# Kernel optimization log

Measured on AMD Instinct MI355X. Metric: run time of the kernel, lower is better.

Reference implementation:

```python
import jax, jax.numpy as jnp
import numpy as np
from jax import lax

# ---- module hyperparams (match init_kwargs and mamba_ssm Mamba2 defaults) ----
D_MODEL = 768
D_STATE = 64
D_CONV = 4
EXPAND = 2
HEADDIM = 64  # Mamba2 default
D_INNER = EXPAND * D_MODEL          # 1536
NHEADS = D_INNER // HEADDIM         # 24
NGROUPS = 1
CONV_DIM = D_INNER + 2 * NGROUPS * D_STATE          # 1664
D_IN_PROJ = 2 * D_INNER + 2 * NGROUPS * D_STATE + NHEADS  # 3224
BSZ, SEQ = 2, 512
EPS = 1e-5


def setup_inputs() -> dict:
    key = jax.random.key(0)
    ks = jax.random.split(key, 12)
    def n(k, shape, s):
        return jax.random.normal(k, shape, jnp.float32) * s
    x = n(ks[0], (BSZ, SEQ, D_MODEL), 1.0)
    in_proj_w = n(ks[1], (D_IN_PROJ, D_MODEL), D_MODEL ** -0.5)
    conv_w = n(ks[2], (CONV_DIM, D_CONV), D_CONV ** -0.5)
    conv_b = jnp.zeros((CONV_DIM,), jnp.float32)
    # dt_bias = softplus^{-1}(dt) with dt log-uniform in [1e-3, 1e-1] (Mamba2 init)
    dt = jnp.exp(jax.random.uniform(ks[3], (NHEADS,), jnp.float32,
                                    minval=np.log(1e-3), maxval=np.log(1e-1)))
    dt_bias = dt + jnp.log(-jnp.expm1(-dt))
    A_log = jnp.log(jax.random.uniform(ks[4], (NHEADS,), jnp.float32, minval=1.0, maxval=16.0))
    D_param = jnp.ones((NHEADS,), jnp.float32)
    norm_w = jnp.ones((D_INNER,), jnp.float32)
    out_proj_w = n(ks[5], (D_MODEL, D_INNER), D_INNER ** -0.5)
    ln1_w = jnp.ones((D_MODEL,), jnp.float32); ln1_b = jnp.zeros((D_MODEL,), jnp.float32)
    ln2_w = jnp.ones((D_MODEL,), jnp.float32); ln2_b = jnp.zeros((D_MODEL,), jnp.float32)
    ff_w1 = n(ks[6], (4 * D_MODEL, D_MODEL), D_MODEL ** -0.5)
    ff_b1 = jnp.zeros((4 * D_MODEL,), jnp.float32)
    ff_w2 = n(ks[7], (D_MODEL, 4 * D_MODEL), (4 * D_MODEL) ** -0.5)
    ff_b2 = jnp.zeros((D_MODEL,), jnp.float32)
    return dict(x=x, in_proj_w=in_proj_w, conv_w=conv_w, conv_b=conv_b,
                dt_bias=dt_bias, A_log=A_log, D_param=D_param, norm_w=norm_w,
                out_proj_w=out_proj_w, ln1_w=ln1_w, ln1_b=ln1_b,
                ln2_w=ln2_w, ln2_b=ln2_b, ff_w1=ff_w1, ff_b1=ff_b1,
                ff_w2=ff_w2, ff_b2=ff_b2)


def layernorm(x, w, b):
    mu = jnp.mean(x, -1, keepdims=True)
    xc = x - mu
    var = jnp.mean(xc * xc, -1, keepdims=True)
    return xc * lax.rsqrt(var + EPS) * w + b


def mamba2(xn, in_proj_w, conv_w, conv_b, dt_bias, A_log, D_param, norm_w, out_proj_w):
    b, l, _ = xn.shape
    zxbcdt = xn @ in_proj_w.T  # [b, l, D_IN_PROJ]
    z = zxbcdt[..., :D_INNER]
    xBC = zxbcdt[..., D_INNER:D_INNER + CONV_DIM]
    dt = zxbcdt[..., D_INNER + CONV_DIM:]
    # causal depthwise conv over time on xBC
    xc = lax.conv_general_dilated(xBC.transpose(0, 2, 1), conv_w[:, None, :], (1,),
                                  [(D_CONV - 1, 0)], dimension_numbers=('NCH', 'OIH', 'NCH'),
                                  feature_group_count=CONV_DIM)
    xBC = jax.nn.silu((xc + conv_b[None, :, None]).transpose(0, 2, 1))
    xs = xBC[..., :D_INNER].reshape(b, l, NHEADS, HEADDIM)
    Bm = xBC[..., D_INNER:D_INNER + D_STATE]   # [b, l, n]  (ngroups=1)
    Cm = xBC[..., D_INNER + D_STATE:]          # [b, l, n]
    dt = jax.nn.softplus(dt + dt_bias)         # [b, l, h]
    dA = jnp.exp(dt * (-jnp.exp(A_log)))       # [b, l, h]
    dBx = jnp.einsum('blh,bln,blhp->blhpn', dt, Bm, xs)
    def step(h, inp):
        dA_t, dBx_t = inp                      # [b,h], [b,h,p,n]
        h = dA_t[:, :, None, None] * h + dBx_t
        return h, h
    _, hs = lax.scan(step, jnp.zeros((b, NHEADS, HEADDIM, D_STATE), xn.dtype),
                     (dA.transpose(1, 0, 2), dBx.transpose(1, 0, 2, 3, 4)))
    y = jnp.einsum('lbhpn,bln->blhp', hs, Cm) + D_param[None, None, :, None] * xs
    y = y.reshape(b, l, D_INNER) * jax.nn.silu(z)   # gated RMSNorm (norm_before_gate=False)
    y = y * lax.rsqrt(jnp.mean(y * y, -1, keepdims=True) + EPS) * norm_w
    return y @ out_proj_w.T


def reference(x, in_proj_w, conv_w, conv_b, dt_bias, A_log, D_param, norm_w,
              out_proj_w, ln1_w, ln1_b, ln2_w, ln2_b, ff_w1, ff_b1, ff_w2, ff_b2):
    residual = x
    xn = layernorm(x, ln1_w, ln1_b)
    mp = (in_proj_w, conv_w, conv_b, dt_bias, A_log, D_param, norm_w, out_proj_w)
    out_f = mamba2(xn, *mp)
    out_b = jnp.flip(mamba2(jnp.flip(xn, 1), *mp), 1)
    m = layernorm(out_f + out_b, ln2_w, ln2_b)
    ff = jax.nn.gelu(m @ ff_w1.T + ff_b1, approximate=False) @ ff_w2.T + ff_b2
    return ff + residual
```

## Files before the change

### kernel.cpp

```cpp
#include <hip/hip_runtime.h>
#include <hip/hip_bf16.h>
#include <math.h>

#define SEQ     512
#define BSZ     2
#define ROWS    (BSZ*SEQ)
#define DMODEL  768
#define DINNER  1536
#define DSTATE  64
#define NHEADS  24
#define HEADDIM 64
#define CONVDIM 1664
#define DINPROJ 3224
#define DFF     3072
#define EPSF    1e-5f

typedef __attribute__((ext_vector_type(8))) short s16x8;
typedef __attribute__((ext_vector_type(4))) float f32x4;

__device__ __forceinline__ float b2f(const __hip_bfloat16 v){ return __bfloat162float(v); }
__device__ __forceinline__ __hip_bfloat16 f2b(float v){ return __float2bfloat16(v); }
__device__ __forceinline__ ushort f2bu(float v){
  union { __hip_bfloat16 b; ushort u; } c; c.b = __float2bfloat16(v); return c.u;
}
__device__ __forceinline__ float u2f(ushort u){ return __uint_as_float(((uint)u) << 16); }

__device__ __forceinline__ void gload16(const void* g, void* l){
  __builtin_amdgcn_global_load_lds((__attribute__((address_space(1))) const void*)g,
                                   (__attribute__((address_space(3))) void*)l, 16, 0, 0);
}

__device__ __forceinline__ float block_sum256(float v, float* sh){
  #pragma unroll
  for (int off = 32; off > 0; off >>= 1) v += __shfl_down(v, off, 64);
  int w = threadIdx.x >> 6;
  if ((threadIdx.x & 63) == 0) sh[w] = v;
  __syncthreads();
  float t = sh[0] + sh[1] + sh[2] + sh[3];
  __syncthreads();
  return t;
}

__global__ __launch_bounds__(256) void zerof_kernel(float* out, int n){
  int i = blockIdx.x*256 + threadIdx.x;
  if (i < n) out[i] = 0.f;
}

__global__ __launch_bounds__(256) void prep_kernel(const float* __restrict__ w0,
    const float* __restrict__ w1, const float* __restrict__ w2,
    const float* __restrict__ w3, ushort* __restrict__ o,
    int n0, int n1, int n2, int n3, int wblocks,
    const float* __restrict__ xin, const float* __restrict__ lnw,
    const float* __restrict__ lnb, __hip_bfloat16* __restrict__ xnout)
{
  __shared__ float sh[4];
  if ((int)blockIdx.x < wblocks){
    int i = (blockIdx.x*256 + threadIdx.x) << 2;
    int total = n0 + n1 + n2 + n3;
    if (i < total){
      const float* s; int off;
      if      (i < n0)       { s = w0; off = i; }
      else if (i < n0+n1)    { s = w1; off = i - n0; }
      else if (i < n0+n1+n2) { s = w2; off = i - n0 - n1; }
      else                   { s = w3; off = i - n0 - n1 - n2; }
      float4 f = *(const float4*)(s + off);
      *(ushort4*)(o + i) = make_ushort4(f2bu(f.x), f2bu(f.y), f2bu(f.z), f2bu(f.w));
    }
    return;
  }
  const int row = blockIdx.x - wblocks;
  const float* xr = xin + (size_t)row * DMODEL;
  float v[3]; float s = 0.f;
  #pragma unroll
  for (int i = 0; i < 3; i++){ int c = threadIdx.x + i*256; v[i] = xr[c]; s += v[i]; }
  s = block_sum256(s, sh);
  float mu = s * (1.f/DMODEL);
  float s2 = 0.f;
  #pragma unroll
  for (int i = 0; i < 3; i++){ float d = v[i]-mu; s2 += d*d; }
  s2 = block_sum256(s2, sh);
  float rs = rsqrtf(s2*(1.f/DMODEL) + EPSF);
  #pragma unroll
  for (int i = 0; i < 3; i++){
    int c = threadIdx.x + i*256;
    xnout[(size_t)row*DMODEL + c] = f2b((v[i]-mu)*rs*lnw[c] + lnb[c]);
  }
}

__global__ __launch_bounds__(256) void ln_kernel(const float* __restrict__ in,
    const float* __restrict__ w, const float* __restrict__ b,
    __hip_bfloat16* __restrict__ out)
{
  __shared__ float sh[4];
  const int row = blockIdx.x;
  const float* xr = in + (size_t)row * DMODEL;
  float v[3]; float s = 0.f;
  #pragma unroll
  for (int i = 0; i < 3; i++){ int c = threadIdx.x + i*256; v[i] = xr[c]; s += v[i]; }
  s = block_sum256(s, sh);
  float mu = s * (1.f/DMODEL);
  float s2 = 0.f;
  #pragma unroll
  for (int i = 0; i < 3; i++){ float d = v[i]-mu; s2 += d*d; }
  s2 = block_sum256(s2, sh);
  float rs = rsqrtf(s2*(1.f/DMODEL) + EPSF);
  #pragma unroll
  for (int i = 0; i < 3; i++){
    int c = threadIdx.x + i*256;
    out[(size_t)row*DMODEL + c] = f2b((v[i]-mu)*rs*w[c] + b[c]);
  }
}

__device__ __forceinline__ s16x8 ld_frag(const ushort* p){
  union { ushort4 h[2]; s16x8 v; } u;
  u.h[0] = *(const ushort4*)(p);
  u.h[1] = *(const ushort4*)(p + 4);
  return u.v;
}

template<typename CTy, int KS, int EPI>
__global__ __launch_bounds__(256) void gemm_bb64(const __hip_bfloat16* __restrict__ A_,
    const __hip_bfloat16* __restrict__ B_, CTy* __restrict__ C,
    const float* __restrict__ bias, int M, int N, int K)
{
  __shared__ __align__(16) ushort As[2][64][64];
  __shared__ __align__(16) ushort Bs[2][64][64];
  const int tid  = threadIdx.x;
  const int lane = tid & 63, wave = tid >> 6;
  const int wr = wave >> 1, wc = wave & 1;
  const int n0 = blockIdx.x * 64, m0 = blockIdx.y * 64;
  const int Kc   = K / KS;
  const int kbeg = blockIdx.z * Kc;
  const int srw  = lane >> 3;
  const int scol = (((lane & 7) ^ srw) << 3);
  const int l15  = lane & 15;
  const int r7   = l15 & 7;
  const int c0   = lane >> 4;

  const ushort* Au = (const ushort*)A_;
  const ushort* Bu = (const ushort*)B_;

  f32x4 acc[2][2] = {};

  auto stage = [&](int bf, int k0){
    #pragma unroll
    for (int q = 0; q < 2; q++){
      int row = q*32 + wave*8 + srw;
      gload16(Au + (size_t)(m0 + row)*K + kbeg + k0 + scol, &As[bf][q*32 + wave*8][0]);
      int nr = n0 + row; if (nr > N-1) nr = N-1;
      gload16(Bu + (size_t)nr*K + kbeg + k0 + scol, &Bs[bf][q*32 + wave*8][0]);
    }
  };

  stage(0, 0);
  __syncthreads();
  int cur = 0;
  for (int k0 = 0; k0 < Kc; k0 += 64){
    if (k0 + 64 < Kc) stage(cur ^ 1, k0 + 64);
    #pragma unroll
    for (int t = 0; t < 2; t++){
      const int fc = (((t*4 + c0) ^ r7) << 3);
      s16x8 a0 = ld_frag(&As[cur][wr*32      + l15][fc]);
      s16x8 a1 = ld_frag(&As[cur][wr*32 + 16 + l15][fc]);
      s16x8 b0 = ld_frag(&Bs[cur][wc*32      + l15][fc]);
      s16x8 b1 = ld_frag(&Bs[cur][wc*32 + 16 + l15][fc]);
      acc[0][0] = __builtin_amdgcn_mfma_f32_16x16x32_bf16(a0, b0, acc[0][0], 0, 0, 0);
      acc[0][1] = __builtin_amdgcn_mfma_f32_16x16x32_bf16(a0, b1, acc[0][1], 0, 0, 0);
      acc[1][0] = __builtin_amdgcn_mfma_f32_16x16x32_bf16(a1, b0, acc[1][0], 0, 0, 0);
      acc[1][1] = __builtin_amdgcn_mfma_f32_16x16x32_bf16(a1, b1, acc[1][1], 0, 0, 0);
    }
    __syncthreads();
    cur ^= 1;
  }

  CTy* Cz = C + (size_t)blockIdx.z * M * N;
  const int crow = (lane >> 4) * 4;
  #pragma unroll
  for (int i = 0; i < 2; i++){
    #pragma unroll
    for (int j = 0; j < 2; j++){
      int col = n0 + wc*32 + j*16 + l15;
      if (col < N){
        #pragma unroll
        for (int q = 0; q < 4; q++){
          int rowg = m0 + wr*32 + i*16 + crow + q;
          if constexpr (EPI == 1){
            float v = acc[i][j][q] + bias[col];
            Cz[(size_t)rowg*N + col] = (CTy)f2b(0.5f * v * (1.f + erff(v * 0.70710678118654752f)));
          } else if constexpr (sizeof(CTy) == 4){
            Cz[(size_t)rowg*N + col] = acc[i][j][q];
          } else {
            Cz[(size_t)rowg*N + col] = (CTy)f2b(acc[i][j][q]);
          }
        }
      }
    }
  }
}

template<typename CTy>
__global__ __launch_bounds__(256) void gemm_mfma(const __hip_bfloat16* __restrict__ A,
    const float* __restrict__ B, CTy* __restrict__ C, int M, int N, int K)
{
  __shared__ __align__(16) ushort As[64][72];
  __shared__ __align__(16) ushort Bs[64][72];
  const int tid  = threadIdx.x;
  const int lane = tid & 63, wave = tid >> 6;
  const int wr = wave >> 1, wc = wave & 1;
  const int n0 = blockIdx.x * 64, m0 = blockIdx.y * 64;
  const int sr = tid >> 2;
  const int sc = (tid & 3) * 16;
  const int l15 = lane & 15, lk = (lane >> 4) * 8;

  f32x4 acc[2][2] = {};

  const ushort* Au = (const ushort*)A;
  int nr = n0 + sr; if (nr > N-1) nr = N-1;

  for (int k0 = 0; k0 < K; k0 += 64){
    const ushort* ag = Au + (size_t)(m0 + sr)*K + (k0 + sc);
    ushort4 a0 = *(const ushort4*)(ag);
    ushort4 a1 = *(const ushort4*)(ag + 4);
    ushort4 a2 = *(const ushort4*)(ag + 8);
    ushort4 a3 = *(const ushort4*)(ag + 12);
    const float* bg = B + (size_t)nr*K + (k0 + sc);
    float4 f0 = *(const float4*)(bg);
    float4 f1 = *(const float4*)(bg + 4);
    float4 f2 = *(const float4*)(bg + 8);
    float4 f3 = *(const float4*)(bg + 12);
    ushort4 b0 = make_ushort4(f2bu(f0.x), f2bu(f0.y), f2bu(f0.z), f2bu(f0.w));
    ushort4 b1 = make_ushort4(f2bu(f1.x), f2bu(f1.y), f2bu(f1.z), f2bu(f1.w));
    ushort4 b2 = make_ushort4(f2bu(f2.x), f2bu(f2.y), f2bu(f2.z), f2bu(f2.w));
    ushort4 b3 = make_ushort4(f2bu(f3.x), f2bu(f3.y), f2bu(f3.z), f2bu(f3.w));

    __syncthreads();
    *(ushort4*)&As[sr][sc +  0] = a0;
    *(ushort4*)&As[sr][sc +  4] = a1;
    *(ushort4*)&As[sr][sc +  8] = a2;
    *(ushort4*)&As[sr][sc + 12] = a3;
    *(ushort4*)&Bs[sr][sc +  0] = b0;
    *(ushort4*)&Bs[sr][sc +  4] = b1;
    *(ushort4*)&Bs[sr][sc +  8] = b2;
    *(ushort4*)&Bs[sr][sc + 12] = b3;
    __syncthreads();

    #pragma unroll
    for (int kk = 0; kk < 64; kk += 32){
      s16x8 af0 = ld_frag(&As[wr*32      + l15][kk + lk]);
      s16x8 af1 = ld_frag(&As[wr*32 + 16 + l15][kk + lk]);
      s16x8 bf0 = ld_frag(&Bs[wc*32      + l15][kk + lk]);
      s16x8 bf1 = ld_frag(&Bs[wc*32 + 16 + l15][kk + lk]);
      acc[0][0] = __builtin_amdgcn_mfma_f32_16x16x32_bf16(af0, bf0, acc[0][0], 0, 0, 0);
      acc[0][1] = __builtin_amdgcn_mfma_f32_16x16x32_bf16(af0, bf1, acc[0][1], 0, 0, 0);
      acc[1][0] = __builtin_amdgcn_mfma_f32_16x16x32_bf16(af1, bf0, acc[1][0], 0, 0, 0);
      acc[1][1] = __builtin_amdgcn_mfma_f32_16x16x32_bf16(af1, bf1, acc[1][1], 0, 0, 0);
    }
  }

  const int crow = (lane >> 4) * 4;
  #pragma unroll
  for (int i = 0; i < 2; i++){
    #pragma unroll
    for (int j = 0; j < 2; j++){
      int col = n0 + wc*32 + j*16 + l15;
      if (col < N){
        #pragma unroll
        for (int q = 0; q < 4; q++){
          int rowg = m0 + wr*32 + i*16 + crow + q;
          if constexpr (sizeof(CTy) == 4) C[(size_t)rowg*N + col] = acc[i][j][q];
          else                            C[(size_t)rowg*N + col] = (CTy)f2b(acc[i][j][q]);
        }
      }
    }
  }
}

__global__ __launch_bounds__(256) void convdt_kernel(const __hip_bfloat16* __restrict__ zx,
    const float* __restrict__ cw, const float* __restrict__ cb,
    const float* __restrict__ dt_bias, const float* __restrict__ A_log,
    __hip_bfloat16* __restrict__ xconv, float* __restrict__ dtb, float* __restrict__ dab)
{
  const int tt = blockIdx.x, b = blockIdx.y, dir = blockIdx.z;
  const int c8 = threadIdx.x * 8;
  if (c8 < CONVDIM){
    size_t rowoff[4]; bool ok[4];
    #pragma unroll
    for (int k = 0; k < 4; k++){
      int s = tt - 3 + k;
      ok[k] = (s >= 0);
      int ss = ok[k] ? s : 0;
      int phys = dir ? (SEQ-1-ss) : ss;
      rowoff[k] = ((size_t)(b*SEQ + phys))*DINPROJ + DINNER + c8;
    }
    float acc[8];
    {
      float4 cb0 = *(const float4*)(cb + c8);
      float4 cb1 = *(const float4*)(cb + c8 + 4);
      acc[0]=cb0.x; acc[1]=cb0.y; acc[2]=cb0.z; acc[3]=cb0.w;
      acc[4]=cb1.x; acc[5]=cb1.y; acc[6]=cb1.z; acc[7]=cb1.w;
    }
    float wv[8][4];
    #pragma unroll
    for (int j = 0; j < 8; j++){
      float4 w4 = *(const float4*)(cw + (size_t)(c8 + j)*4);
      wv[j][0]=w4.x; wv[j][1]=w4.y; wv[j][2]=w4.z; wv[j][3]=w4.w;
    }
    const ushort* zu = (const ushort*)zx;
    #pragma unroll
    for (int k = 0; k < 4; k++){
      if (ok[k]){
        ushort4 v0 = *(const ushort4*)(zu + rowoff[k]);
        ushort4 v1 = *(const ushort4*)(zu + rowoff[k] + 4);
        acc[0] = fmaf(wv[0][k], u2f(v0.x), acc[0]);
        acc[1] = fmaf(wv[1][k], u2f(v0.y), acc[1]);
        acc[2] = fmaf(wv[2][k], u2f(v0.z), acc[2]);
        acc[3] = fmaf(wv[3][k], u2f(v0.w), acc[3]);
        acc[4] = fmaf(wv[4][k], u2f(v1.x), acc[4]);
        acc[5] = fmaf(wv[5][k], u2f(v1.y), acc[5]);
        acc[6] = fmaf(wv[6][k], u2f(v1.z), acc[6]);
        acc[7] = fmaf(wv[7][k], u2f(v1.w), acc[7]);
      }
    }
    ushort* outr = (ushort*)xconv + ((size_t)((dir*BSZ + b)*SEQ + tt))*CONVDIM + c8;
    ushort o[8];
    #pragma unroll
    for (int j = 0; j < 8; j++){
      float s = acc[j] / (1.f + expf(-acc[j]));
      o[j] = f2bu(s);
    }
    *(ushort4*)(outr)     = make_ushort4(o[0],o[1],o[2],o[3]);
    *(ushort4*)(outr + 4) = make_ushort4(o[4],o[5],o[6],o[7]);
  }
  if (dir == 0 && threadIdx.x < NHEADS){
    int h = threadIdx.x;
    size_t r = (size_t)b*SEQ + tt;
    float raw = b2f(zx[r*DINPROJ + (DINNER + CONVDIM) + h]) + dt_bias[h];
    float sp  = fmaxf(raw, 0.f) + log1pf(expf(-fabsf(raw)));
    dtb[r*NHEADS + h] = sp;
    dab[r*NHEADS + h] = expf(-sp * expf(A_log[h]));
  }
}

#define CT 16

__global__ __launch_bounds__(256) void scan_pass1(const __hip_bfloat16* __restrict__ xconv,
    const float* __restrict__ dtb, const float* __restrict__ dab,
    float* __restrict__ stateBuf, int CL)
{
  const int c = blockIdx.x, h = blockIdx.y, z = blockIdx.z;
  const int b = z & 1, dir = z >> 1;
  const int tid = threadIdx.x, lane = tid & 63, wave = tid >> 6, nb = wave * 16;
  __shared__ __align__(16) float Bc[CT][64], Xc[CT][64];
  __shared__ float dAc[CT], dtc[CT];
  float hreg[16];
  #pragma unroll
  for (int j = 0; j < 16; j++) hreg[j] = 0.f;
  const size_t dirbase = (size_t)z * SEQ;
  const int cstart = c * CL;

  const int ttl = tid >> 4, c4 = (tid & 15) << 2;

  for (int c0 = cstart; c0 < cstart + CL; c0 += CT){
    {
      const ushort* rowp = (const ushort*)xconv + (dirbase + c0 + ttl)*(size_t)CONVDIM;
      ushort4 bv = *(const ushort4*)(rowp + DINNER + c4);
      ushort4 xv = *(const ushort4*)(rowp + h*HEADDIM + c4);
      Bc[ttl][c4+0] = u2f(bv.x); Bc[ttl][c4+1] = u2f(bv.y);
      Bc[ttl][c4+2] = u2f(bv.z); Bc[ttl][c4+3] = u2f(bv.w);
      Xc[ttl][c4+0] = u2f(xv.x); Xc[ttl][c4+1] = u2f(xv.y);
      Xc[ttl][c4+2] = u2f(xv.z); Xc[ttl][c4+3] = u2f(xv.w);
    }
    if (tid < CT){
      int phys = dir ? (SEQ-1 - (c0 + tid)) : (c0 + tid);
      size_t r = (size_t)b*SEQ + phys;
      dAc[tid] = dab[r*NHEADS + h];
      dtc[tid] = dtb[r*NHEADS + h];
    }
    __syncthreads();

    #pragma unroll 4
    for (int tt = 0; tt < CT; tt++){
      float dA = dAc[tt];
      float dtx = dtc[tt] * Xc[tt][lane];
      const float4* Bq = (const float4*)&Bc[tt][nb];
      float4 B0 = Bq[0], B1 = Bq[1], B2 = Bq[2], B3 = Bq[3];
      hreg[ 0]=fmaf(dA,hreg[ 0],dtx*B0.x); hreg[ 1]=fmaf(dA,hreg[ 1],dtx*B0.y);
      hreg[ 2]=fmaf(dA,hreg[ 2],dtx*B0.z); hreg[ 3]=fmaf(dA,hreg[ 3],dtx*B0.w);
      hreg[ 4]=fmaf(dA,hreg[ 4],dtx*B1.x); hreg[ 5]=fmaf(dA,hreg[ 5],dtx*B1.y);
      hreg[ 6]=fmaf(dA,hreg[ 6],dtx*B1.z); hreg[ 7]=fmaf(dA,hreg[ 7],dtx*B1.w);
      hreg[ 8]=fmaf(dA,hreg[ 8],dtx*B2.x); hreg[ 9]=fmaf(dA,hreg[ 9],dtx*B2.y);
      hreg[10]=fmaf(dA,hreg[10],dtx*B2.z); hreg[11]=fmaf(dA,hreg[11],dtx*B2.w);
      hreg[12]=fmaf(dA,hreg[12],dtx*B3.x); hreg[13]=fmaf(dA,hreg[13],dtx*B3.y);
      hreg[14]=fmaf(dA,hreg[14],dtx*B3.z); hreg[15]=fmaf(dA,hreg[15],dtx*B3.w);
    }
    __syncthreads();
  }

  float* sp = stateBuf + (((size_t)c*4 + z)*NHEADS + h)*4096 + (size_t)lane*64 + nb;
  *(float4*)(sp +  0) = make_float4(hreg[ 0],hreg[ 1],hreg[ 2],hreg[ 3]);
  *(float4*)(sp +  4) = make_float4(hreg[ 4],hreg[ 5],hreg[ 6],hreg[ 7]);
  *(float4*)(sp +  8) = make_float4(hreg[ 8],hreg[ 9],hreg[10],hreg[11]);
  *(float4*)(sp + 12) = make_float4(hreg[12],hreg[13],hreg[14],hreg[15]);
}

__global__ __launch_bounds__(256) void scan_fixup(const float* __restrict__ dab,
    float* __restrict__ stateBuf, int NC, int CL)
{
  const int h = blockIdx.x, z = blockIdx.y;
  const int b = z & 1, dir = z >> 1;
  const int tid = threadIdx.x;
  __shared__ float sdA[SEQ];
  __shared__ float P[8];
  for (int i = tid; i < SEQ; i += 256){
    int phys = dir ? (SEQ-1-i) : i;
    sdA[i] = dab[((size_t)b*SEQ + phys)*NHEADS + h];
  }
  __syncthreads();
  if (tid < NC){
    float p = 1.f;
    for (int i = 0; i < CL; i++) p *= sdA[tid*CL + i];
    P[tid] = p;
  }
  __syncthreads();

  float hrun[16], Lcur[16];
  #pragma unroll
  for (int j = 0; j < 16; j++) hrun[j] = 0.f;
  {
    const float* s0 = stateBuf + ((size_t)z*NHEADS + h)*4096 + (size_t)tid*16;
    #pragma unroll
    for (int j = 0; j < 16; j++) Lcur[j] = s0[j];
  }
  for (int c = 1; c < NC; c++){
    float Pp = P[c-1];
    float hnew[16];
    #pragma unroll
    for (int j = 0; j < 16; j++) hnew[j] = fmaf(Pp, hrun[j], Lcur[j]);
    float* sc = stateBuf + (((size_t)c*4 + z)*NHEADS + h)*4096 + (size_t)tid*16;
    if (c < NC-1){
      #pragma unroll
      for (int j = 0; j < 16; j++) Lcur[j] = sc[j];
    }
    #pragma unroll
    for (int j = 0; j < 16; j++) sc[j] = hnew[j];
    #pragma unroll
    for (int j = 0; j < 16; j++) hrun[j] = hnew[j];
  }
}

__global__ __launch_bounds__(256) void scan_pass2(const __hip_bfloat16* __restrict__ xconv,
    const __hip_bfloat16* __restrict__ zx, const float* __restrict__ dtb,
    const float* __restrict__ dab, const float* __restrict__ Dp,
    const float* __restrict__ stateBuf, __hip_bfloat16* __restrict__ yg, int CL)
{
  const int c = blockIdx.x, h = blockIdx.y, z = blockIdx.z;
  const int b = z & 1, dir = z >> 1;
  const int tid = threadIdx.x, lane = tid & 63, wave = tid >> 6, nb = wave * 16;
  __shared__ __align__(16) float Bc[CT][64], Cc[CT][64], Xc[CT][64];
  __shared__ __align__(16) float Yp[4][CT][64];
  __shared__ float dAc[CT], dtc[CT];
  float hreg[16];
  if (c == 0){
    #pragma unroll
    for (int j = 0; j < 16; j++) hreg[j] = 0.f;
  } else {
    const float* sp = stateBuf + (((size_t)c*4 + z)*NHEADS + h)*4096 + (size_t)lane*64 + nb;
    float4 s0 = *(const float4*)(sp+0), s1 = *(const float4*)(sp+4);
    float4 s2 = *(const float4*)(sp+8), s3 = *(const float4*)(sp+12);
    hreg[ 0]=s0.x; hreg[ 1]=s0.y; hreg[ 2]=s0.z; hreg[ 3]=s0.w;
    hreg[ 4]=s1.x; hreg[ 5]=s1.y; hreg[ 6]=s1.z; hreg[ 7]=s1.w;
    hreg[ 8]=s2.x; hreg[ 9]=s2.y; hreg[10]=s2.z; hreg[11]=s2.w;
    hreg[12]=s3.x; hreg[13]=s3.y; hreg[14]=s3.z; hreg[15]=s3.w;
  }
  const float Dh = Dp[h];
  const size_t dirbase = (size_t)z * SEQ;
  const int cstart = c * CL;
  const int ttl = tid >> 4, c4 = (tid & 15) << 2;

  for (int c0 = cstart; c0 < cstart + CL; c0 += CT){
    {
      const ushort* rowp = (const ushort*)xconv + (dirbase + c0 + ttl)*(size_t)CONVDIM;
      ushort4 bv = *(const ushort4*)(rowp + DINNER + c4);
      ushort4 cv = *(const ushort4*)(rowp + DINNER + DSTATE + c4);
      ushort4 xv = *(const ushort4*)(rowp + h*HEADDIM + c4);
      Bc[ttl][c4+0] = u2f(bv.x); Bc[ttl][c4+1] = u2f(bv.y);
      Bc[ttl][c4+2] = u2f(bv.z); Bc[ttl][c4+3] = u2f(bv.w);
      Cc[ttl][c4+0] = u2f(cv.x); Cc[ttl][c4+1] = u2f(cv.y);
      Cc[ttl][c4+2] = u2f(cv.z); Cc[ttl][c4+3] = u2f(cv.w);
      Xc[ttl][c4+0] = u2f(xv.x); Xc[ttl][c4+1] = u2f(xv.y);
      Xc[ttl][c4+2] = u2f(xv.z); Xc[ttl][c4+3] = u2f(xv.w);
    }
    if (tid < CT){
      int phys = dir ? (SEQ-1 - (c0 + tid)) : (c0 + tid);
      size_t r = (size_t)b*SEQ + phys;
      dAc[tid] = dab[r*NHEADS + h];
      dtc[tid] = dtb[r*NHEADS + h];
    }
    __syncthreads();

    #pragma unroll 4
    for (int tt = 0; tt < CT; tt++){
      float dA = dAc[tt];
      float dtx = dtc[tt] * Xc[tt][lane];
      const float4* Bq = (const float4*)&Bc[tt][nb];
      const float4* Cq = (const float4*)&Cc[tt][nb];
      float4 B0 = Bq[0], B1 = Bq[1], B2 = Bq[2], B3 = Bq[3];
      float4 C0 = Cq[0], C1 = Cq[1], C2 = Cq[2], C3 = Cq[3];
      float y0 = 0.f, y1 = 0.f, y2 = 0.f, y3 = 0.f;
      hreg[ 0]=fmaf(dA,hreg[ 0],dtx*B0.x); y0=fmaf(hreg[ 0],C0.x,y0);
      hreg[ 1]=fmaf(dA,hreg[ 1],dtx*B0.y); y1=fmaf(hreg[ 1],C0.y,y1);
      hreg[ 2]=fmaf(dA,hreg[ 2],dtx*B0.z); y2=fmaf(hreg[ 2],C0.z,y2);
      hreg[ 3]=fmaf(dA,hreg[ 3],dtx*B0.w); y3=fmaf(hreg[ 3],C0.w,y3);
      hreg[ 4]=fmaf(dA,hreg[ 4],dtx*B1.x); y0=fmaf(hreg[ 4],C1.x,y0);
      hreg[ 5]=fmaf(dA,hreg[ 5],dtx*B1.y); y1=fmaf(hreg[ 5],C1.y,y1);
      hreg[ 6]=fmaf(dA,hreg[ 6],dtx*B1.z); y2=fmaf(hreg[ 6],C1.z,y2);
      hreg[ 7]=fmaf(dA,hreg[ 7],dtx*B1.w); y3=fmaf(hreg[ 7],C1.w,y3);
      hreg[ 8]=fmaf(dA,hreg[ 8],dtx*B2.x); y0=fmaf(hreg[ 8],C2.x,y0);
      hreg[ 9]=fmaf(dA,hreg[ 9],dtx*B2.y); y1=fmaf(hreg[ 9],C2.y,y1);
      hreg[10]=fmaf(dA,hreg[10],dtx*B2.z); y2=fmaf(hreg[10],C2.z,y2);
      hreg[11]=fmaf(dA,hreg[11],dtx*B2.w); y3=fmaf(hreg[11],C2.w,y3);
      hreg[12]=fmaf(dA,hreg[12],dtx*B3.x); y0=fmaf(hreg[12],C3.x,y0);
      hreg[13]=fmaf(dA,hreg[13],dtx*B3.y); y1=fmaf(hreg[13],C3.y,y1);
      hreg[14]=fmaf(dA,hreg[14],dtx*B3.z); y2=fmaf(hreg[14],C3.z,y2);
      hreg[15]=fmaf(dA,hreg[15],dtx*B3.w); y3=fmaf(hreg[15],C3.w,y3);
      Yp[wave][tt][lane] = (y0+y1) + (y2+y3);
    }
    __syncthreads();

    {
      int tl = tid >> 4, p4 = (tid & 15) << 2;
      float4 ya = *(const float4*)&Yp[0][tl][p4];
      float4 yb4 = *(const float4*)&Yp[1][tl][p4];
      float4 yc = *(const float4*)&Yp[2][tl][p4];
      float4 yd = *(const float4*)&Yp[3][tl][p4];
      float4 xv = *(const float4*)&Xc[tl][p4];
      int phys = dir ? (SEQ-1 - (c0 + tl)) : (c0 + tl);
      size_t r = (size_t)b*SEQ + phys;
      const ushort* zp = (const ushort*)zx + r*DINPROJ + h*HEADDIM + p4;
      ushort4 zv = *(const ushort4*)zp;
      float zf[4] = { u2f(zv.x), u2f(zv.y), u2f(zv.z), u2f(zv.w) };
      float yv[4] = { ya.x+yb4.x+yc.x+yd.x + Dh*xv.x,
                      ya.y+yb4.y+yc.y+yd.y + Dh*xv.y,
                      ya.z+yb4.z+yc.z+yd.z + Dh*xv.z,
                      ya.w+yb4.w+yc.w+yd.w + Dh*xv.w };
      ushort o[4];
      #pragma unroll
      for (int j = 0; j < 4; j++){
        float sil = zf[j] / (1.f + expf(-zf[j]));
        o[j] = f2bu(yv[j] * sil);
      }
      ushort* op = (ushort*)yg + ((size_t)dir*ROWS + r)*DINNER + h*HEADDIM + p4;
      *(ushort4*)op = make_ushort4(o[0],o[1],o[2],o[3]);
    }
    __syncthreads();
  }
}

__global__ __launch_bounds__(256) void rmscomb_kernel(const __hip_bfloat16* __restrict__ yg,
    const float* __restrict__ nw, __hip_bfloat16* __restrict__ u)
{
  __shared__ float sh[4];
  const int row = blockIdx.x;
  const __hip_bfloat16* yf = yg + (size_t)row*DINNER;
  const __hip_bfloat16* yb = yg + (size_t)(ROWS + row)*DINNER;
  float vf[6], vb[6]; float sf = 0.f, sb = 0.f;
  #pragma unroll
  for (int i = 0; i < 6; i++){
    int c = threadIdx.x + i*256;
    vf[i] = b2f(yf[c]); sf += vf[i]*vf[i];
    vb[i] = b2f(yb[c]); sb += vb[i]*vb[i];
  }
  sf = block_sum256(sf, sh);
  sb = block_sum256(sb, sh);
  float rf = rsqrtf(sf*(1.f/DINNER) + EPSF);
  float rb = rsqrtf(sb*(1.f/DINNER) + EPSF);
  #pragma unroll
  for (int i = 0; i < 6; i++){
    int c = threadIdx.x + i*256;
    u[(size_t)row*DINNER + c] = f2b((vf[i]*rf + vb[i]*rb) * nw[c]);
  }
}

template<int NP>
__global__ __launch_bounds__(256) void ln2_kernel(const float* __restrict__ in,
    size_t pstride, const float* __restrict__ w, const float* __restrict__ b,
    __hip_bfloat16* __restrict__ out)
{
  __shared__ float sh[4];
  const int row = blockIdx.x;
  float v[3]; float s = 0.f;
  #pragma unroll
  for (int i = 0; i < 3; i++){
    int c = threadIdx.x + i*256;
    size_t idx = (size_t)row*DMODEL + c;
    float t = 0.f;
    #pragma unroll
    for (int p = 0; p < NP; p++) t += in[p*pstride + idx];
    v[i] = t; s += t;
  }
  s = block_sum256(s, sh);
  float mu = s * (1.f/DMODEL);
  float s2 = 0.f;
  #pragma unroll
  for (int i = 0; i < 3; i++){ float d = v[i]-mu; s2 += d*d; }
  s2 = block_sum256(s2, sh);
  float rs = rsqrtf(s2*(1.f/DMODEL) + EPSF);
  #pragma unroll
  for (int i = 0; i < 3; i++){
    int c = threadIdx.x + i*256;
    out[(size_t)row*DMODEL + c] = f2b((v[i]-mu)*rs*w[c] + b[c]);
  }
}

__global__ __launch_bounds__(256) void gelu_kernel(const __hip_bfloat16* __restrict__ g,
    const float* __restrict__ b1, __hip_bfloat16* __restrict__ out)
{
  size_t idx = (size_t)blockIdx.x*256 + threadIdx.x;
  int c = (int)(idx % DFF);
  float v = b2f(g[idx]) + b1[c];
  out[idx] = f2b(0.5f * v * (1.f + erff(v * 0.70710678118654752f)));
}

template<int NP>
__global__ __launch_bounds__(256) void final_kernel(const float* __restrict__ f,
    size_t pstride, const float* __restrict__ bias, const float* __restrict__ x,
    float* __restrict__ out)
{
  size_t i4 = ((size_t)blockIdx.x*256 + threadIdx.x) << 2;
  int c = (int)(i4 % DMODEL);
  float4 bv = *(const float4*)(bias + c);
  float4 xv = *(const float4*)(x + i4);
  float4 s = make_float4(bv.x+xv.x, bv.y+xv.y, bv.z+xv.z, bv.w+xv.w);
  #pragma unroll
  for (int p = 0; p < NP; p++){
    float4 fv = *(const float4*)(f + p*pstride + i4);
    s.x += fv.x; s.y += fv.y; s.z += fv.z; s.w += fv.w;
  }
  *(float4*)(out + i4) = s;
}

extern "C" void kernel_launch(void* const* d_in, const int* in_sizes, int n_in,
                              void* d_out, int out_size, void* d_ws, size_t ws_size,
                              hipStream_t stream)
{
  float* out = (float*)d_out;

  const size_t NEED = 19906560;
  if (ws_size < NEED || n_in < 17){
    zerof_kernel<<<(out_size + 255)/256, 256, 0, stream>>>(out, out_size);
    return;
  }

  const float* x       = (const float*)d_in[0];
  const float* in_proj_w = (const float*)d_in[1];
  const float* conv_w  = (const float*)d_in[2];
  const float* conv_b  = (const float*)d_in[3];
  const float* dt_bias = (const float*)d_in[4];
  const float* A_log   = (const float*)d_in[5];
  const float* D_param = (const float*)d_in[6];
  const float* norm_w  = (const float*)d_in[7];
  const float* out_proj_w = (const float*)d_in[8];
  const float* ln1_w   = (const float*)d_in[9];
  const float* ln1_b   = (const float*)d_in[10];
  const float* ln2_w   = (const float*)d_in[11];
  const float* ln2_b   = (const float*)d_in[12];
  const float* ff_w1   = (const float*)d_in[13];
  const float* ff_b1   = (const float*)d_in[14];
  const float* ff_w2   = (const float*)d_in[15];
  const float* ff_b2   = (const float*)d_in[16];

  char* ws = (char*)d_ws;
  __hip_bfloat16* zx  = (__hip_bfloat16*)(ws + 0);
  __hip_bfloat16* xn  = (__hip_bfloat16*)(ws + 6602752);
  float*          dtb = (float*)(ws + 6602752);
  float*          dab = (float*)(ws + 6701056);
  __hip_bfloat16* xcv = (__hip_bfloat16*)(ws + 6799360);
  __hip_bfloat16* yg  = (__hip_bfloat16*)(ws + 13615104);
  __hip_bfloat16* u   = (__hip_bfloat16*)(ws + 0);
  float*          mo  = (float*)(ws + 3145728);
  __hip_bfloat16* mb  = (__hip_bfloat16*)(ws + 0);
  __hip_bfloat16* g   = (__hip_bfloat16*)(ws + 6799360);
  __hip_bfloat16* gb  = (__hip_bfloat16*)(ws + 13615104);
  float*          fo  = (float*)(ws + 0);

  const size_t WBALL = 16748544;
  const size_t PARTS = 12582912;
  const size_t CHB   = 1572864;
  const size_t PSTRIDE = (size_t)ROWS * DMODEL;
  const int WN_IN  = DINPROJ*DMODEL;
  const int WN_OUT = DMODEL*DINNER;
  const int WN_F1  = DFF*DMODEL;
  const int WN_F2  = DMODEL*DFF;

  size_t rem = ws_size - NEED;
  bool fast = (rem >= WBALL + PARTS);
  ushort* wb    = (ushort*)(ws + NEED);
  float*  parts = (float*) (ws + NEED + WBALL);
  size_t scanoff = NEED + (fast ? (WBALL + PARTS) : 0);
  size_t srem = ws_size - scanoff;
  int NC = 1;
  if      (srem >= 8*CHB) NC = 8;
  else if (srem >= 4*CHB) NC = 4;
  else if (srem >= 2*CHB) NC = 2;
  float* stateBuf = (float*)(ws + scanoff);
  const int CL = SEQ / NC;

  if (fast){
    const int wblocks = (WN_IN + WN_OUT + WN_F1 + WN_F2) / 4 / 256;
    prep_kernel<<<wblocks + ROWS, 256, 0, stream>>>(in_proj_w, out_proj_w, ff_w1, ff_w2,
        wb, WN_IN, WN_OUT, WN_F1, WN_F2, wblocks, x, ln1_w, ln1_b, xn);
    gemm_bb64<__hip_bfloat16,1,0><<<dim3((DINPROJ+63)/64, ROWS/64), 256, 0, stream>>>(
        xn, (const __hip_bfloat16*)wb, zx, nullptr, ROWS, DINPROJ, DMODEL);
  } else {
    ln_kernel<<<ROWS, 256, 0, stream>>>(x, ln1_w, ln1_b, xn);
    gemm_mfma<<<dim3((DINPROJ+63)/64, ROWS/64), 256, 0, stream>>>(xn, in_proj_w, zx, ROWS, DINPROJ, DMODEL);
  }
  convdt_kernel<<<dim3(SEQ, BSZ, 2), 256, 0, stream>>>(zx, conv_w, conv_b, dt_bias, A_log, xcv, dtb, dab);
  if (NC > 1){
    scan_pass1<<<dim3(NC-1, NHEADS, 4), 256, 0, stream>>>(xcv, dtb, dab, stateBuf, CL);
    scan_fixup<<<dim3(NHEADS, 4), 256, 0, stream>>>(dab, stateBuf, NC, CL);
  }
  scan_pass2<<<dim3(NC, NHEADS, 4), 256, 0, stream>>>(xcv, zx, dtb, dab, D_param, stateBuf, yg, CL);
  rmscomb_kernel<<<ROWS, 256, 0, stream>>>(yg, norm_w, u);
  if (fast){
    gemm_bb64<float,2,0><<<dim3(DMODEL/64, ROWS/64, 2), 256, 0, stream>>>(
        u, (const __hip_bfloat16*)(wb + WN_IN), parts, nullptr, ROWS, DMODEL, DINNER);
    ln2_kernel<2><<<ROWS, 256, 0, stream>>>(parts, PSTRIDE, ln2_w, ln2_b, mb);
  } else {
    gemm_mfma<<<dim3(DMODEL/64, ROWS/64), 256, 0, stream>>>(u, out_proj_w, mo, ROWS, DMODEL, DINNER);
    ln2_kernel<1><<<ROWS, 256, 0, stream>>>(mo, 0, ln2_w, ln2_b, mb);
  }
  if (fast){
    gemm_bb64<__hip_bfloat16,1,1><<<dim3(DFF/64, ROWS/64), 256, 0, stream>>>(
        mb, (const __hip_bfloat16*)(wb + WN_IN + WN_OUT), gb, ff_b1, ROWS, DFF, DMODEL);
  } else {
    gemm_mfma<<<dim3(DFF/64, ROWS/64), 256, 0, stream>>>(mb, ff_w1, g, ROWS, DFF, DMODEL);
    gelu_kernel<<<(ROWS*DFF)/256, 256, 0, stream>>>(g, ff_b1, gb);
  }
  if (fast){
    gemm_bb64<float,4,0><<<dim3(DMODEL/64, ROWS/64, 4), 256, 0, stream>>>(
        gb, (const __hip_bfloat16*)(wb + WN_IN + WN_OUT + WN_F1), parts, nullptr, ROWS, DMODEL, DFF);
    final_kernel<4><<<(ROWS*DMODEL/4)/256, 256, 0, stream>>>(parts, PSTRIDE, ff_b2, x, out);
  } else {
    gemm_mfma<<<dim3(DMODEL/64, ROWS/64), 256, 0, stream>>>(gb, ff_w2, fo, ROWS, DMODEL, DFF);
    final_kernel<1><<<(ROWS*DMODEL/4)/256, 256, 0, stream>>>(fo, 0, ff_b2, x, out);
  }
}
```

Before: 250.5 us.

## Double-buffer scan chunk loads to overlap global fetches with recurrence

Both scan passes now use double-buffered shared-memory tiles. The next CT-step chunk of B, C, X, z, dA and dt is loaded into registers from global memory before the current chunk's recurrence runs, then written to the alternate buffer afterwards. The aim is to hide global-load latency behind the serial state-update arithmetic and to drop one barrier per chunk in pass1. In exchange, shared memory and register pressure go up, which may reduce occupancy.

Result: faster. 243.5 us (median of 2 runs) (-2.8%).

```diff
diff --git a/kernel.cpp b/kernel.cpp
--- a/kernel.cpp
+++ b/kernel.cpp
@@ -350,39 +350,57 @@
   const int c = blockIdx.x, h = blockIdx.y, z = blockIdx.z;
   const int b = z & 1, dir = z >> 1;
   const int tid = threadIdx.x, lane = tid & 63, wave = tid >> 6, nb = wave * 16;
-  __shared__ __align__(16) float Bc[CT][64], Xc[CT][64];
-  __shared__ float dAc[CT], dtc[CT];
+  __shared__ __align__(16) float Bc[2][CT][64], Xc[2][CT][64];
+  __shared__ float dAc[2][CT], dtc[2][CT];
   float hreg[16];
   #pragma unroll
   for (int j = 0; j < 16; j++) hreg[j] = 0.f;
   const size_t dirbase = (size_t)z * SEQ;
   const int cstart = c * CL;
-
   const int ttl = tid >> 4, c4 = (tid & 15) << 2;
-
-  for (int c0 = cstart; c0 < cstart + CL; c0 += CT){
-    {
-      const ushort* rowp = (const ushort*)xconv + (dirbase + c0 + ttl)*(size_t)CONVDIM;
-      ushort4 bv = *(const ushort4*)(rowp + DINNER + c4);
-      ushort4 xv = *(const ushort4*)(rowp + h*HEADDIM + c4);
-      Bc[ttl][c4+0] = u2f(bv.x); Bc[ttl][c4+1] = u2f(bv.y);
-      Bc[ttl][c4+2] = u2f(bv.z); Bc[ttl][c4+3] = u2f(bv.w);
-      Xc[ttl][c4+0] = u2f(xv.x); Xc[ttl][c4+1] = u2f(xv.y);
-      Xc[ttl][c4+2] = u2f(xv.z); Xc[ttl][c4+3] = u2f(xv.w);
-    }
+  const int nt = CL / CT;
+
+  ushort4 cb_, cx_; float cda = 0.f, cdt = 0.f;
+  {
+    const ushort* rowp = (const ushort*)xconv + (dirbase + cstart + ttl)*(size_t)CONVDIM;
+    cb_ = *(const ushort4*)(rowp + DINNER + c4);
+    cx_ = *(const ushort4*)(rowp + h*HEADDIM + c4);
     if (tid < CT){
-      int phys = dir ? (SEQ-1 - (c0 + tid)) : (c0 + tid);
+      int phys = dir ? (SEQ-1 - (cstart + tid)) : (cstart + tid);
       size_t r = (size_t)b*SEQ + phys;
-      dAc[tid] = dab[r*NHEADS + h];
-      dtc[tid] = dtb[r*NHEADS + h];
-    }
-    __syncthreads();
+      cda = dab[r*NHEADS + h];
+      cdt = dtb[r*NHEADS + h];
+    }
+  }
+  Bc[0][ttl][c4+0]=u2f(cb_.x); Bc[0][ttl][c4+1]=u2f(cb_.y);
+  Bc[0][ttl][c4+2]=u2f(cb_.z); Bc[0][ttl][c4+3]=u2f(cb_.w);
+  Xc[0][ttl][c4+0]=u2f(cx_.x); Xc[0][ttl][c4+1]=u2f(cx_.y);
+  Xc[0][ttl][c4+2]=u2f(cx_.z); Xc[0][ttl][c4+3]=u2f(cx_.w);
+  if (tid < CT){ dAc[0][tid]=cda; dtc[0][tid]=cdt; }
+  __syncthreads();
+
+  int cur = 0;
+  for (int it = 0; it < nt; ++it){
+    ushort4 nb_, nx_; float nda = 0.f, ndt = 0.f;
+    const bool more = (it+1 < nt);
+    if (more){
+      int c0n = cstart + (it+1)*CT;
+      const ushort* rowp = (const ushort*)xconv + (dirbase + c0n + ttl)*(size_t)CONVDIM;
+      nb_ = *(const ushort4*)(rowp + DINNER + c4);
+      nx_ = *(const ushort4*)(rowp + h*HEADDIM + c4);
+      if (tid < CT){
+        int phys = dir ? (SEQ-1 - (c0n + tid)) : (c0n + tid);
+        size_t r = (size_t)b*SEQ + phys;
+        nda = dab[r*NHEADS + h];
+        ndt = dtb[r*NHEADS + h];
+      }
+    }
 
     #pragma unroll 4
     for (int tt = 0; tt < CT; tt++){
-      float dA = dAc[tt];
-      float dtx = dtc[tt] * Xc[tt][lane];
-      const float4* Bq = (const float4*)&Bc[tt][nb];
+      float dA = dAc[cur][tt];
+      float dtx = dtc[cur][tt] * Xc[cur][tt][lane];
+      const float4* Bq = (const float4*)&Bc[cur][tt][nb];
       float4 B0 = Bq[0], B1 = Bq[1], B2 = Bq[2], B3 = Bq[3];
       hreg[ 0]=fmaf(dA,hreg[ 0],dtx*B0.x); hreg[ 1]=fmaf(dA,hreg[ 1],dtx*B0.y);
       hreg[ 2]=fmaf(dA,hreg[ 2],dtx*B0.z); hreg[ 3]=fmaf(dA,hreg[ 3],dtx*B0.w);
@@ -393,7 +411,17 @@
       hreg[12]=fmaf(dA,hreg[12],dtx*B3.x); hreg[13]=fmaf(dA,hreg[13],dtx*B3.y);
       hreg[14]=fmaf(dA,hreg[14],dtx*B3.z); hreg[15]=fmaf(dA,hreg[15],dtx*B3.w);
     }
+
+    if (more){
+      int nxt = cur ^ 1;
+      Bc[nxt][ttl][c4+0]=u2f(nb_.x); Bc[nxt][ttl][c4+1]=u2f(nb_.y);
+      Bc[nxt][ttl][c4+2]=u2f(nb_.z); Bc[nxt][ttl][c4+3]=u2f(nb_.w);
+      Xc[nxt][ttl][c4+0]=u2f(nx_.x); Xc[nxt][ttl][c4+1]=u2f(nx_.y);
+      Xc[nxt][ttl][c4+2]=u2f(nx_.z); Xc[nxt][ttl][c4+3]=u2f(nx_.w);
+      if (tid < CT){ dAc[nxt][tid]=nda; dtc[nxt][tid]=ndt; }
+    }
     __syncthreads();
+    cur ^= 1;
   }
 
   float* sp = stateBuf + (((size_t)c*4 + z)*NHEADS + h)*4096 + (size_t)lane*64 + nb;
@@ -456,9 +484,9 @@
   const int c = blockIdx.x, h = blockIdx.y, z = blockIdx.z;
   const int b = z & 1, dir = z >> 1;
   const int tid = threadIdx.x, lane = tid & 63, wave = tid >> 6, nb = wave * 16;
-  __shared__ __align__(16) float Bc[CT][64], Cc[CT][64], Xc[CT][64];
+  __shared__ __align__(16) float Bc[2][CT][64], Cc[2][CT][64], Xc[2][CT][64];
   __shared__ __align__(16) float Yp[4][CT][64];
-  __shared__ float dAc[CT], dtc[CT];
+  __shared__ float dAc[2][CT], dtc[2][CT];
   float hreg[16];
   if (c == 0){
     #pragma unroll
@@ -476,34 +504,60 @@
   const size_t dirbase = (size_t)z * SEQ;
   const int cstart = c * CL;
   const int ttl = tid >> 4, c4 = (tid & 15) << 2;
-
-  for (int c0 = cstart; c0 < cstart + CL; c0 += CT){
-    {
-      const ushort* rowp = (const ushort*)xconv + (dirbase + c0 + ttl)*(size_t)CONVDIM;
-      ushort4 bv = *(const ushort4*)(rowp + DINNER + c4);
-      ushort4 cv = *(const ushort4*)(rowp + DINNER + DSTATE + c4);
-      ushort4 xv = *(const ushort4*)(rowp + h*HEADDIM + c4);
-      Bc[ttl][c4+0] = u2f(bv.x); Bc[ttl][c4+1] = u2f(bv.y);
-      Bc[ttl][c4+2] = u2f(bv.z); Bc[ttl][c4+3] = u2f(bv.w);
-      Cc[ttl][c4+0] = u2f(cv.x); Cc[ttl][c4+1] = u2f(cv.y);
-      Cc[ttl][c4+2] = u2f(cv.z); Cc[ttl][c4+3] = u2f(cv.w);
-      Xc[ttl][c4+0] = u2f(xv.x); Xc[ttl][c4+1] = u2f(xv.y);
-      Xc[ttl][c4+2] = u2f(xv.z); Xc[ttl][c4+3] = u2f(xv.w);
-    }
+  const int nt = CL / CT;
+
+  ushort4 cb_, cc_, cx_, cz_; float cda = 0.f, cdt = 0.f;
+  {
+    const ushort* rowp = (const ushort*)xconv + (dirbase + cstart + ttl)*(size_t)CONVDIM;
+    cb_ = *(const ushort4*)(rowp + DINNER + c4);
+    cc_ = *(const ushort4*)(rowp + DINNER + DSTATE + c4);
+    cx_ = *(const ushort4*)(rowp + h*HEADDIM + c4);
+    int physz = dir ? (SEQ-1 - (cstart + ttl)) : (cstart + ttl);
+    size_t rz = (size_t)b*SEQ + physz;
+    cz_ = *(const ushort4*)((const ushort*)zx + rz*DINPROJ + h*HEADDIM + c4);
     if (tid < CT){
-      int phys = dir ? (SEQ-1 - (c0 + tid)) : (c0 + tid);
+      int phys = dir ? (SEQ-1 - (cstart + tid)) : (cstart + tid);
       size_t r = (size_t)b*SEQ + phys;
-      dAc[tid] = dab[r*NHEADS + h];
-      dtc[tid] = dtb[r*NHEADS + h];
-    }
-    __syncthreads();
+      cda = dab[r*NHEADS + h];
+      cdt = dtb[r*NHEADS + h];
+    }
+  }
+  Bc[0][ttl][c4+0]=u2f(cb_.x); Bc[0][ttl][c4+1]=u2f(cb_.y);
+  Bc[0][ttl][c4+2]=u2f(cb_.z); Bc[0][ttl][c4+3]=u2f(cb_.w);
+  Cc[0][ttl][c4+0]=u2f(cc_.x); Cc[0][ttl][c4+1]=u2f(cc_.y);
+  Cc[0][ttl][c4+2]=u2f(cc_.z); Cc[0][ttl][c4+3]=u2f(cc_.w);
+  Xc[0][ttl][c4+0]=u2f(cx_.x); Xc[0][ttl][c4+1]=u2f(cx_.y);
+  Xc[0][ttl][c4+2]=u2f(cx_.z); Xc[0][ttl][c4+3]=u2f(cx_.w);
+  if (tid < CT){ dAc[0][tid]=cda; dtc[0][tid]=cdt; }
+  __syncthreads();
+
+  int cur = 0;
+  for (int it = 0; it < nt; ++it){
+    ushort4 nb_, nc_, nx_, nz_; float nda = 0.f, ndt = 0.f;
+    const bool more = (it+1 < nt);
+    if (more){
+      int c0n = cstart + (it+1)*CT;
+      const ushort* rowp = (const ushort*)xconv + (dirbase + c0n + ttl)*(size_t)CONVDIM;
+      nb_ = *(const ushort4*)(rowp + DINNER + c4);
+      nc_ = *(const ushort4*)(rowp + DINNER + DSTATE + c4);
+      nx_ = *(const ushort4*)(rowp + h*HEADDIM + c4);
+      int physz = dir ? (SEQ-1 - (c0n + ttl)) : (c0n + ttl);
+      size_t rz = (size_t)b*SEQ + physz;
+      nz_ = *(const ushort4*)((const ushort*)zx + rz*DINPROJ + h*HEADDIM + c4);
+      if (tid < CT){
+        int phys = dir ? (SEQ-1 - (c0n + tid)) : (c0n + tid);
+        size_t r = (size_t)b*SEQ + phys;
+        nda = dab[r*NHEADS + h];
+        ndt = dtb[r*NHEADS + h];
+      }
+    }
 
     #pragma unroll 4
     for (int tt = 0; tt < CT; tt++){
-      float dA = dAc[tt];
-      float dtx = dtc[tt] * Xc[tt][lane];
-      const float4* Bq = (const float4*)&Bc[tt][nb];
-      const float4* Cq = (const float4*)&Cc[tt][nb];
+      float dA = dAc[cur][tt];
+      float dtx = dtc[cur][tt] * Xc[cur][tt][lane];
+      const float4* Bq = (const float4*)&Bc[cur][tt][nb];
+      const float4* Cq = (const float4*)&Cc[cur][tt][nb];
       float4 B0 = Bq[0], B1 = Bq[1], B2 = Bq[2], B3 = Bq[3];
       float4 C0 = Cq[0], C1 = Cq[1], C2 = Cq[2], C3 = Cq[3];
       float y0 = 0.f, y1 = 0.f, y2 = 0.f, y3 = 0.f;
@@ -527,18 +581,27 @@
     }
     __syncthreads();
 
+    if (more){
+      int nxt = cur ^ 1;
+      Bc[nxt][ttl][c4+0]=u2f(nb_.x); Bc[nxt][ttl][c4+1]=u2f(nb_.y);
+      Bc[nxt][ttl][c4+2]=u2f(nb_.z); Bc[nxt][ttl][c4+3]=u2f(nb_.w);
+      Cc[nxt][ttl][c4+0]=u2f(nc_.x); Cc[nxt][ttl][c4+1]=u2f(nc_.y);
+      Cc[nxt][ttl][c4+2]=u2f(nc_.z); Cc[nxt][ttl][c4+3]=u2f(nc_.w);
+      Xc[nxt][ttl][c4+0]=u2f(nx_.x); Xc[nxt][ttl][c4+1]=u2f(nx_.y);
+      Xc[nxt][ttl][c4+2]=u2f(nx_.z); Xc[nxt][ttl][c4+3]=u2f(nx_.w);
+      if (tid < CT){ dAc[nxt][tid]=nda; dtc[nxt][tid]=ndt; }
+    }
+
     {
-      int tl = tid >> 4, p4 = (tid & 15) << 2;
-      float4 ya = *(const float4*)&Yp[0][tl][p4];
+      int tl = ttl, p4 = c4;
+      float4 ya  = *(const float4*)&Yp[0][tl][p4];
       float4 yb4 = *(const float4*)&Yp[1][tl][p4];
-      float4 yc = *(const float4*)&Yp[2][tl][p4];
-      float4 yd = *(const float4*)&Yp[3][tl][p4];
-      float4 xv = *(const float4*)&Xc[tl][p4];
-      int phys = dir ? (SEQ-1 - (c0 + tl)) : (c0 + tl);
+      float4 yc  = *(const float4*)&Yp[2][tl][p4];
+      float4 yd  = *(const float4*)&Yp[3][tl][p4];
+      float4 xv  = *(const float4*)&Xc[cur][tl][p4];
+      int phys = dir ? (SEQ-1 - (cstart + it*CT + tl)) : (cstart + it*CT + tl);
       size_t r = (size_t)b*SEQ + phys;
-      const ushort* zp = (const ushort*)zx + r*DINPROJ + h*HEADDIM + p4;
-      ushort4 zv = *(const ushort4*)zp;
-      float zf[4] = { u2f(zv.x), u2f(zv.y), u2f(zv.z), u2f(zv.w) };
+      float zf[4] = { u2f(cz_.x), u2f(cz_.y), u2f(cz_.z), u2f(cz_.w) };
       float yv[4] = { ya.x+yb4.x+yc.x+yd.x + Dh*xv.x,
                       ya.y+yb4.y+yc.y+yd.y + Dh*xv.y,
                       ya.z+yb4.z+yc.z+yd.z + Dh*xv.z,
@@ -553,6 +616,8 @@
       *(ushort4*)op = make_ushort4(o[0],o[1],o[2],o[3]);
     }
     __syncthreads();
+    if (more) cz_ = nz_;
+    cur ^= 1;
   }
 }
 
```
